# Optimization experiments

Measured on AMD Instinct MI355X. Metric: run time of the kernel, lower is better.

Reference implementation:

```python
import jax, jax.numpy as jnp
import numpy as np

BETA = 0.99  # EMA momentum from init_kwargs
EPS = 1e-12  # torch F.normalize eps


def _normalize(v):
    # matches torch.nn.functional.normalize (L2, dim=-1, eps clamp)
    n = jnp.maximum(jnp.linalg.norm(v, axis=-1, keepdims=True), EPS)
    return v / n


def setup_inputs() -> dict:
    key = jax.random.key(0)
    k1, k2 = jax.random.split(key)
    x = jax.random.normal(k1, (16384, 1024), dtype=jnp.float32)
    group_features = jax.random.uniform(k2, (8192, 1024), dtype=jnp.float32)
    return {"x": x, "group_features": group_features}


def reference(x, group_features):
    n_groups = group_features.shape[0]
    # assign_groups: cosine-sim argmax (normalized copies; does NOT modify x used below)
    xn = _normalize(x)
    gn = _normalize(group_features)
    logits = xn @ gn.T                      # [B, G]
    assignments = jnp.argmax(logits, axis=-1)  # [B] int

    # bincount over groups
    counts = jax.ops.segment_sum(
        jnp.ones_like(assignments, dtype=jnp.int32), assignments, num_segments=n_groups
    )  # [G]

    # scale only groups that received at least one sample by beta
    gf = jnp.where((counts > 0)[:, None], group_features * BETA, group_features)

    # scatter-add EMA contribution: (1-beta) * mean-style sum of raw x per group
    per_sample = x / counts[assignments][:, None].astype(x.dtype)  # safe: count>=1 for assigned
    contrib = jax.ops.segment_sum(per_sample, assignments, num_segments=n_groups)  # [G, D]
    gf = gf + (1.0 - BETA) * contrib

    return _normalize(gf)
```

## Files before the change

### kernel.cpp

```cpp
#include <hip/hip_runtime.h>
#include <float.h>

#define B_N 16384
#define G_N 8192
#define D_N 1024
#define NT 96

typedef unsigned short u16;
typedef unsigned long long u64;
typedef __attribute__((ext_vector_type(8))) short short8;
typedef __attribute__((ext_vector_type(16))) float f32x16;

#define AS1 __attribute__((address_space(1)))
#define AS3 __attribute__((address_space(3)))


__global__ __launch_bounds__(256) void k_norms(const float* __restrict__ g,
                                               float* __restrict__ invn) {
    const int j = blockIdx.x;
    const int t = threadIdx.x;
    const float4 v = *reinterpret_cast<const float4*>(&g[(size_t)j * D_N + t * 4]);
    float s = v.x * v.x + v.y * v.y + v.z * v.z + v.w * v.w;
#pragma unroll
    for (int off = 32; off >= 1; off >>= 1) s += __shfl_down(s, off, 64);
    __shared__ float wsum[4];
    if ((t & 63) == 0) wsum[t >> 6] = s;
    __syncthreads();
    if (t == 0) {
        const float tot = wsum[0] + wsum[1] + wsum[2] + wsum[3];
        invn[j] = 1.0f / fmaxf(sqrtf(tot), 1e-12f);
    }
}

__global__ void k_counts(const u64* __restrict__ pk, int* __restrict__ counts) {
    const int i = blockIdx.x * blockDim.x + threadIdx.x;
    if (i < B_N) {
        const int a = 8191 - (int)(pk[i] & 0x1FFFull);
        atomicAdd(&counts[a], 1);
    }
}

__global__ __launch_bounds__(256) void k_scatter(const float* __restrict__ x,
                                                 const u64* __restrict__ pk,
                                                 const int* __restrict__ counts,
                                                 float* __restrict__ contrib) {
    const int i = blockIdx.x;
    const int a = 8191 - (int)(pk[i] & 0x1FFFull);
    const float scale = 1.0f / (float)counts[a];
    const int t = threadIdx.x;
    const float4 v = *reinterpret_cast<const float4*>(&x[(size_t)i * D_N + t * 4]);
    float* dst = &contrib[(size_t)a * D_N + t * 4];
    atomicAdd(dst + 0, v.x * scale);
    atomicAdd(dst + 1, v.y * scale);
    atomicAdd(dst + 2, v.z * scale);
    atomicAdd(dst + 3, v.w * scale);
}

__global__ __launch_bounds__(256) void k_finalize(const float* __restrict__ g,
                                                  const int* __restrict__ counts,
                                                  float* __restrict__ out) {
    const int j = blockIdx.x;
    const int t = threadIdx.x;
    const float sc = (counts[j] > 0) ? 0.99f : 1.0f;
    const float4 gv = *reinterpret_cast<const float4*>(&g[(size_t)j * D_N + t * 4]);
    const float4 cv = *reinterpret_cast<const float4*>(&out[(size_t)j * D_N + t * 4]);
    float4 gf;
    gf.x = sc * gv.x + 0.01f * cv.x;
    gf.y = sc * gv.y + 0.01f * cv.y;
    gf.z = sc * gv.z + 0.01f * cv.z;
    gf.w = sc * gv.w + 0.01f * cv.w;
    float s = gf.x * gf.x + gf.y * gf.y + gf.z * gf.z + gf.w * gf.w;
#pragma unroll
    for (int off = 32; off >= 1; off >>= 1) s += __shfl_down(s, off, 64);
    __shared__ float wsum[4];
    __shared__ float s_inv;
    if ((t & 63) == 0) wsum[t >> 6] = s;
    __syncthreads();
    if (t == 0) s_inv = 1.0f / fmaxf(sqrtf(wsum[0] + wsum[1] + wsum[2] + wsum[3]), 1e-12f);
    __syncthreads();
    gf.x *= s_inv; gf.y *= s_inv; gf.z *= s_inv; gf.w *= s_inv;
    *reinterpret_cast<float4*>(&out[(size_t)j * D_N + t * 4]) = gf;
}


__device__ inline u16 f2bf_rtn(float f) {
    unsigned u = __float_as_uint(f);
    unsigned r = u + 0x7fffu + ((u >> 16) & 1u);
    return (u16)(r >> 16);
}
__device__ inline float bf2f(u16 h) { return __uint_as_float(((unsigned)h) << 16); }

__global__ __launch_bounds__(256) void k_split(const float* __restrict__ src,
                                               u16* __restrict__ hi,
                                               u16* __restrict__ lo) {
    const size_t i4 = (size_t)blockIdx.x * 256 + threadIdx.x;
    const float4 v = *reinterpret_cast<const float4*>(&src[i4 * 4]);
    u16 h[4], l[4];
    const float f[4] = {v.x, v.y, v.z, v.w};
#pragma unroll
    for (int j = 0; j < 4; ++j) {
        h[j] = f2bf_rtn(f[j]);
        l[j] = f2bf_rtn(f[j] - bf2f(h[j]));
    }
    *reinterpret_cast<ushort4*>(&hi[i4 * 4]) = make_ushort4(h[0], h[1], h[2], h[3]);
    *reinterpret_cast<ushort4*>(&lo[i4 * 4]) = make_ushort4(l[0], l[1], l[2], l[3]);
}


#define PHASE(T, BUF, SBUF) do {                                                          \
    const u16* base = lds + (BUF) * 16384;                                                \
    short8 afr[4][2], bfr[2][2];                                                          \
    _Pragma("unroll")                                                                     \
    for (int m = 0; m < 4; ++m) {                                                         \
        afr[m][0] = *reinterpret_cast<const short8*>(base + arow + m * 1024 + aoffk0);    \
        afr[m][1] = *reinterpret_cast<const short8*>(base + arow + m * 1024 + aoffk1);    \
    }                                                                                     \
    _Pragma("unroll")                                                                     \
    for (int n = 0; n < 2; ++n) {                                                         \
        bfr[n][0] = *reinterpret_cast<const short8*>(base + brow + n * 1024 + aoffk0);    \
        bfr[n][1] = *reinterpret_cast<const short8*>(base + brow + n * 1024 + aoffk1);    \
    }                                                                                     \
    STG((T) + 2, SBUF);                                                                   \
    __builtin_amdgcn_s_setprio(1);                                                        \
    _Pragma("unroll")                                                                     \
    for (int ks = 0; ks < 2; ++ks)                                                        \
        _Pragma("unroll")                                                                 \
        for (int m = 0; m < 4; ++m)                                                       \
            _Pragma("unroll")                                                             \
            for (int n = 0; n < 2; ++n)                                                   \
                acc[m][n] = __builtin_amdgcn_mfma_f32_32x32x16_bf16(                      \
                    afr[m][ks], bfr[n][ks], acc[m][n], 0, 0, 0);                          \
    __builtin_amdgcn_s_setprio(0);                                                        \
    asm volatile("s_waitcnt vmcnt(4)" ::: "memory");                                      \
    __builtin_amdgcn_s_barrier();                                                         \
} while (0)

__global__ __launch_bounds__(512, 2) void k_gemm_argmax(
    const u16* __restrict__ x_hi, const u16* __restrict__ x_lo,
    const u16* __restrict__ g_hi, const u16* __restrict__ g_lo,
    const float* __restrict__ invn, u64* __restrict__ pk) {

    __shared__ __align__(16) u16 lds[49152];

    const int bid = blockIdx.x;
    const int xcd = bid & 7, lcl = bid >> 3;
    const int mblk = xcd * 8 + ((lcl >> 3) & 7);
    const int nblk = (lcl & 7) + (lcl >> 6) * 8;
    const int mrow0 = mblk * 256, nrow0 = nblk * 256;

    const int tid = threadIdx.x;
    const int lane = tid & 63;
    const int w = tid >> 6;
    const int wr = w >> 2, wc = w & 3;

    const int l31 = lane & 31, l5 = lane >> 5;
    const int xq = (lane >> 1) & 3;
    const int arow = (wr * 128 + l31) * 32;
    const int brow = 8192 + (wc * 64 + l31) * 32;
    const int aoffk0 = ((0 + l5) ^ xq) * 8;
    const int aoffk1 = ((2 + l5) ^ xq) * 8;

    const int r0 = tid >> 2;
    const int xsl = (tid & 3) ^ ((tid >> 3) & 3);
    const size_t sA = (size_t)(mrow0 + r0) * D_N + xsl * 8;
    const size_t sB = (size_t)(nrow0 + r0) * D_N + xsl * 8;
    const int dstc = (tid & 448) * 8;

    auto STG = [&](int T, int buf3) {
        const int Tc = T < NT ? T : NT - 1;
        const int term = Tc >> 5;
        const u16* xb = (term == 1) ? x_lo : x_hi;
        const u16* gb = (term == 2) ? g_lo : g_hi;
        const int ko = (Tc & 31) * 32;
        u16* da = lds + buf3 * 16384;
        u16* db = da + 8192;
        __builtin_amdgcn_global_load_lds((const AS1 void*)(xb + sA + ko),          (AS3 void*)(da + dstc), 16, 0, 0);
        __builtin_amdgcn_global_load_lds((const AS1 void*)(xb + sA + 131072 + ko), (AS3 void*)(da + 4096 + dstc), 16, 0, 0);
        __builtin_amdgcn_global_load_lds((const AS1 void*)(gb + sB + ko),          (AS3 void*)(db + dstc), 16, 0, 0);
        __builtin_amdgcn_global_load_lds((const AS1 void*)(gb + sB + 131072 + ko), (AS3 void*)(db + 4096 + dstc), 16, 0, 0);
    };

    f32x16 acc[4][2];
#pragma unroll
    for (int m = 0; m < 4; ++m)
#pragma unroll
        for (int n = 0; n < 2; ++n)
#pragma unroll
            for (int r = 0; r < 16; ++r) acc[m][n][r] = 0.0f;

    STG(0, 0); STG(1, 1);
    asm volatile("s_waitcnt vmcnt(4)" ::: "memory");
    __builtin_amdgcn_s_barrier();

    for (int it = 0; it < 32; ++it) {
        const int T = it * 3;
        PHASE(T,     0, 2);
        PHASE(T + 1, 1, 0);
        PHASE(T + 2, 2, 1);
    }

    float inv[2];
    inv[0] = invn[nrow0 + wc * 64 + l31];
    inv[1] = invn[nrow0 + wc * 64 + 32 + l31];

#pragma unroll
    for (int m = 0; m < 4; ++m) {
#pragma unroll
        for (int r = 0; r < 16; ++r) {
            u64 p = 0;
#pragma unroll
            for (int n = 0; n < 2; ++n) {
                const float v = acc[m][n][r] * inv[n];
                unsigned u = __float_as_uint(v);
                u ^= (u >> 31) ? 0xFFFFFFFFu : 0x80000000u;
                const int col = nrow0 + wc * 64 + n * 32 + l31;
                const u64 cand = ((u64)u << 13) | (unsigned)(8191 - col);
                p = (cand > p) ? cand : p;
            }
#pragma unroll
            for (int msk = 1; msk < 32; msk <<= 1) {
                const u64 o = __shfl_xor(p, msk, 64);
                p = (o > p) ? o : p;
            }
            if (l31 == 0) {
                const int row = mrow0 + wr * 128 + m * 32 + (r & 3) + 8 * (r >> 2) + 4 * l5;
                atomicMax(&pk[row], p);
            }
        }
    }
}


__global__ __launch_bounds__(256) void k_argmax_fp32(const float* __restrict__ x,
                                                     const float* __restrict__ g,
                                                     const float* __restrict__ invn,
                                                     int* __restrict__ assign) {
    __shared__ __align__(16) float As[32][68];
    __shared__ __align__(16) float Bs[32][68];
    const int t = threadIdx.x;
    const int tx = t & 15;
    const int ty = t >> 4;
    const int row0 = blockIdx.x * 64;
    const int r_a = t >> 3;
    const int c4 = t & 7;
    float bestv[4]; int besti[4];
#pragma unroll
    for (int i = 0; i < 4; ++i) { bestv[i] = -3.0e38f; besti[i] = 0; }
    for (int jt = 0; jt < G_N / 64; ++jt) {
        float acc[4][4] = {};
        for (int kt = 0; kt < D_N / 32; ++kt) {
#pragma unroll
            for (int p = 0; p < 2; ++p) {
                const int r = r_a + p * 32;
                const float4 va = *reinterpret_cast<const float4*>(&x[(size_t)(row0 + r) * D_N + kt * 32 + c4 * 4]);
                As[c4 * 4 + 0][r] = va.x; As[c4 * 4 + 1][r] = va.y; As[c4 * 4 + 2][r] = va.z; As[c4 * 4 + 3][r] = va.w;
                const float4 vb = *reinterpret_cast<const float4*>(&g[(size_t)(jt * 64 + r) * D_N + kt * 32 + c4 * 4]);
                Bs[c4 * 4 + 0][r] = vb.x; Bs[c4 * 4 + 1][r] = vb.y; Bs[c4 * 4 + 2][r] = vb.z; Bs[c4 * 4 + 3][r] = vb.w;
            }
            __syncthreads();
#pragma unroll
            for (int k = 0; k < 32; ++k) {
                const float4 a = *reinterpret_cast<const float4*>(&As[k][ty * 4]);
                const float4 b = *reinterpret_cast<const float4*>(&Bs[k][tx * 4]);
                const float av[4] = {a.x, a.y, a.z, a.w};
                const float bv[4] = {b.x, b.y, b.z, b.w};
#pragma unroll
                for (int i = 0; i < 4; ++i)
#pragma unroll
                    for (int jj = 0; jj < 4; ++jj) acc[i][jj] += av[i] * bv[jj];
            }
            __syncthreads();
        }
#pragma unroll
        for (int jj = 0; jj < 4; ++jj) {
            const int col = jt * 64 + tx * 4 + jj;
            const float s = invn[col];
#pragma unroll
            for (int i = 0; i < 4; ++i) {
                const float v = acc[i][jj] * s;
                if (v > bestv[i]) { bestv[i] = v; besti[i] = col; }
            }
        }
    }
#pragma unroll
    for (int m = 1; m < 16; m <<= 1) {
#pragma unroll
        for (int i = 0; i < 4; ++i) {
            const float ov = __shfl_xor(bestv[i], m, 64);
            const int oi = __shfl_xor(besti[i], m, 64);
            if (ov > bestv[i] || (ov == bestv[i] && oi < besti[i])) { bestv[i] = ov; besti[i] = oi; }
        }
    }
    if (tx == 0) {
#pragma unroll
        for (int i = 0; i < 4; ++i) assign[row0 + ty * 4 + i] = besti[i];
    }
}

__global__ void k_counts_i(const int* __restrict__ assign, int* __restrict__ counts) {
    const int i = blockIdx.x * blockDim.x + threadIdx.x;
    if (i < B_N) atomicAdd(&counts[assign[i]], 1);
}

__global__ __launch_bounds__(256) void k_scatter_i(const float* __restrict__ x,
                                                   const int* __restrict__ assign,
                                                   const int* __restrict__ counts,
                                                   float* __restrict__ contrib) {
    const int i = blockIdx.x;
    const int a = assign[i];
    const float scale = 1.0f / (float)counts[a];
    const int t = threadIdx.x;
    const float4 v = *reinterpret_cast<const float4*>(&x[(size_t)i * D_N + t * 4]);
    float* dst = &contrib[(size_t)a * D_N + t * 4];
    atomicAdd(dst + 0, v.x * scale);
    atomicAdd(dst + 1, v.y * scale);
    atomicAdd(dst + 2, v.z * scale);
    atomicAdd(dst + 3, v.w * scale);
}


extern "C" void kernel_launch(void* const* d_in, const int* in_sizes, int n_in,
                              void* d_out, int out_size, void* d_ws, size_t ws_size,
                              hipStream_t stream) {
    const float* x = (const float*)d_in[0];
    const float* g = (const float*)d_in[1];
    float* out = (float*)d_out;

    char* ws = (char*)d_ws;
    u16*  x_hi  = (u16*)(ws);
    u16*  x_lo  = (u16*)(ws + 33554432);
    u16*  g_hi  = (u16*)(ws + 67108864);
    u16*  g_lo  = (u16*)(ws + 83886080);
    float* invn = (float*)(ws + 100663296);
    int* counts = (int*)(ws + 100696064);
    u64*   pk   = (u64*)(ws + 100728832);
    const size_t need = 100859904;

    hipMemsetAsync(out, 0, (size_t)G_N * D_N * sizeof(float), stream);

    if (ws_size >= need) {
        hipMemsetAsync(counts, 0, (size_t)G_N * sizeof(int), stream);
        hipMemsetAsync(pk, 0, (size_t)B_N * sizeof(u64), stream);
        k_norms<<<G_N, 256, 0, stream>>>(g, invn);
        k_split<<<B_N * D_N / 4 / 256, 256, 0, stream>>>(x, x_hi, x_lo);
        k_split<<<G_N * D_N / 4 / 256, 256, 0, stream>>>(g, g_hi, g_lo);
        k_gemm_argmax<<<2048, 512, 0, stream>>>(x_hi, x_lo, g_hi, g_lo, invn, pk);
        k_counts<<<B_N / 256, 256, 0, stream>>>(pk, counts);
        k_scatter<<<B_N, 256, 0, stream>>>(x, pk, counts, out);
        k_finalize<<<G_N, 256, 0, stream>>>(g, counts, out);
    } else {
        float* invn_f = (float*)ws;
        int* assign_f = (int*)(ws + (size_t)G_N * 4);
        int* counts_f = (int*)(ws + (size_t)(G_N + B_N) * 4);
        hipMemsetAsync(counts_f, 0, (size_t)G_N * sizeof(int), stream);
        k_norms<<<G_N, 256, 0, stream>>>(g, invn_f);
        k_argmax_fp32<<<B_N / 64, 256, 0, stream>>>(x, g, invn_f, assign_f);
        k_counts_i<<<B_N / 256, 256, 0, stream>>>(assign_f, counts_f);
        k_scatter_i<<<B_N, 256, 0, stream>>>(x, assign_f, counts_f, out);
        k_finalize<<<G_N, 256, 0, stream>>>(g, counts_f, out);
    }
}
```

Before: 1.107 ms.

## Pre-pack bf16 split operands into MFMA fragment order and double-buffer register reads

The hi/lo bf16 split kernel now writes its output in 32-row by 32-k bricks already arranged in MFMA lane order. Each GEMM tile stage can then be fetched with contiguous 16-byte loads, and LDS fragment reads need no swizzle arithmetic. The main loop is restructured to read fragments for the next stage into a second register set while the current stage's MFMAs run. It now waits on vmcnt(0) before each barrier, which trades some prefetch slack for the overlap and uses more registers.

```diff
diff --git a/kernel.cpp b/kernel.cpp
--- a/kernel.cpp
+++ b/kernel.cpp
@@ -1,5 +1,4 @@
 #include <hip/hip_runtime.h>
-#include <float.h>
 
 #define B_N 16384
 #define G_N 8192
@@ -90,49 +89,65 @@
 }
 __device__ inline float bf2f(u16 h) { return __uint_as_float(((unsigned)h) << 16); }
 
-__global__ __launch_bounds__(256) void k_split(const float* __restrict__ src,
-                                               u16* __restrict__ hi,
-                                               u16* __restrict__ lo) {
-    const size_t i4 = (size_t)blockIdx.x * 256 + threadIdx.x;
-    const float4 v = *reinterpret_cast<const float4*>(&src[i4 * 4]);
-    u16 h[4], l[4];
-    const float f[4] = {v.x, v.y, v.z, v.w};
-#pragma unroll
-    for (int j = 0; j < 4; ++j) {
-        h[j] = f2bf_rtn(f[j]);
-        l[j] = f2bf_rtn(f[j] - bf2f(h[j]));
-    }
-    *reinterpret_cast<ushort4*>(&hi[i4 * 4]) = make_ushort4(h[0], h[1], h[2], h[3]);
-    *reinterpret_cast<ushort4*>(&lo[i4 * 4]) = make_ushort4(l[0], l[1], l[2], l[3]);
-}
-
-
-#define PHASE(T, BUF, SBUF) do {                                                          \
-    const u16* base = lds + (BUF) * 16384;                                                \
-    short8 afr[4][2], bfr[2][2];                                                          \
-    _Pragma("unroll")                                                                     \
-    for (int m = 0; m < 4; ++m) {                                                         \
-        afr[m][0] = *reinterpret_cast<const short8*>(base + arow + m * 1024 + aoffk0);    \
-        afr[m][1] = *reinterpret_cast<const short8*>(base + arow + m * 1024 + aoffk1);    \
-    }                                                                                     \
-    _Pragma("unroll")                                                                     \
-    for (int n = 0; n < 2; ++n) {                                                         \
-        bfr[n][0] = *reinterpret_cast<const short8*>(base + brow + n * 1024 + aoffk0);    \
-        bfr[n][1] = *reinterpret_cast<const short8*>(base + brow + n * 1024 + aoffk1);    \
-    }                                                                                     \
-    STG((T) + 2, SBUF);                                                                   \
-    __builtin_amdgcn_s_setprio(1);                                                        \
-    _Pragma("unroll")                                                                     \
-    for (int ks = 0; ks < 2; ++ks)                                                        \
-        _Pragma("unroll")                                                                 \
-        for (int m = 0; m < 4; ++m)                                                       \
-            _Pragma("unroll")                                                             \
-            for (int n = 0; n < 2; ++n)                                                   \
-                acc[m][n] = __builtin_amdgcn_mfma_f32_32x32x16_bf16(                      \
-                    afr[m][ks], bfr[n][ks], acc[m][n], 0, 0, 0);                          \
-    __builtin_amdgcn_s_setprio(0);                                                        \
-    asm volatile("s_waitcnt vmcnt(4)" ::: "memory");                                      \
-    __builtin_amdgcn_s_barrier();                                                         \
+__global__ __launch_bounds__(256) void k_split_pack(const float* __restrict__ src,
+                                                    u16* __restrict__ hi,
+                                                    u16* __restrict__ lo) {
+    const int id = blockIdx.x * 256 + threadIdx.x;
+    const int brick = id >> 7, c = id & 127;
+    const int mu = brick >> 5, tau = brick & 31;
+    const int ks = c >> 6, lane = c & 63;
+    const int row = mu * 32 + (lane & 31);
+    const int k = tau * 32 + ks * 16 + (lane >> 5) * 8;
+    const float* s = src + (size_t)row * D_N + k;
+    const float4 v0 = *reinterpret_cast<const float4*>(s);
+    const float4 v1 = *reinterpret_cast<const float4*>(s + 4);
+    const float f[8] = {v0.x, v0.y, v0.z, v0.w, v1.x, v1.y, v1.z, v1.w};
+    short8 h, l;
+#pragma unroll
+    for (int j = 0; j < 8; ++j) {
+        const u16 hj = f2bf_rtn(f[j]);
+        h[j] = (short)hj;
+        l[j] = (short)f2bf_rtn(f[j] - bf2f(hj));
+    }
+    *reinterpret_cast<short8*>(hi + (size_t)id * 8) = h;
+    *reinterpret_cast<short8*>(lo + (size_t)id * 8) = l;
+}
+
+
+#define MFMA_BLK(S) do {                                                                   \
+    __builtin_amdgcn_s_setprio(1);                                                         \
+    _Pragma("unroll")                                                                      \
+    for (int ks = 0; ks < 2; ++ks)                                                         \
+        _Pragma("unroll")                                                                  \
+        for (int m = 0; m < 4; ++m)                                                        \
+            _Pragma("unroll")                                                              \
+            for (int n = 0; n < 2; ++n)                                                    \
+                acc[m][n] = __builtin_amdgcn_mfma_f32_32x32x16_bf16(                       \
+                    afr[S][m][ks], bfr[S][n][ks], acc[m][n], 0, 0, 0);                     \
+    __builtin_amdgcn_s_setprio(0);                                                         \
+} while (0)
+
+#define READS(BUF, S) do {                                                                 \
+    const u16* aB = lds + (BUF) * 16384 + aRd;                                             \
+    const u16* bB = lds + (BUF) * 16384 + 8192 + bRd;                                      \
+    _Pragma("unroll")                                                                      \
+    for (int m = 0; m < 4; ++m)                                                            \
+        _Pragma("unroll")                                                                  \
+        for (int ks = 0; ks < 2; ++ks)                                                     \
+            afr[S][m][ks] = *reinterpret_cast<const short8*>(aB + m * 1024 + ks * 512);    \
+    _Pragma("unroll")                                                                      \
+    for (int n = 0; n < 2; ++n)                                                            \
+        _Pragma("unroll")                                                                  \
+        for (int ks = 0; ks < 2; ++ks)                                                     \
+            bfr[S][n][ks] = *reinterpret_cast<const short8*>(bB + n * 1024 + ks * 512);    \
+} while (0)
+
+#define BODY(P, BSTG, BRD, SM, SR) do {                                                    \
+    asm volatile("s_waitcnt vmcnt(0)" ::: "memory");                                       \
+    __builtin_amdgcn_s_barrier();                                                          \
+    STG((P) + 2, BSTG);                                                                    \
+    READS(BRD, SR);                                                                        \
+    MFMA_BLK(SM);                                                                          \
 } while (0)
 
 __global__ __launch_bounds__(512, 2) void k_gemm_argmax(
@@ -152,32 +167,29 @@
     const int lane = tid & 63;
     const int w = tid >> 6;
     const int wr = w >> 2, wc = w & 3;
-
     const int l31 = lane & 31, l5 = lane >> 5;
-    const int xq = (lane >> 1) & 3;
-    const int arow = (wr * 128 + l31) * 32;
-    const int brow = 8192 + (wc * 64 + l31) * 32;
-    const int aoffk0 = ((0 + l5) ^ xq) * 8;
-    const int aoffk1 = ((2 + l5) ^ xq) * 8;
-
-    const int r0 = tid >> 2;
-    const int xsl = (tid & 3) ^ ((tid >> 3) & 3);
-    const size_t sA = (size_t)(mrow0 + r0) * D_N + xsl * 8;
-    const size_t sB = (size_t)(nrow0 + r0) * D_N + xsl * 8;
-    const int dstc = (tid & 448) * 8;
-
-    auto STG = [&](int T, int buf3) {
+
+    const int aRd = (wr * 512 + lane) * 8;
+    const int bRd = (wc * 256 + lane) * 8;
+
+    const int wub = (tid & 448) * 8;
+    const int cOff = (tid & 127) * 8;
+    const int brkA = tid >> 7;
+    const size_t aBase = ((size_t)(mblk * 8 + brkA)) * 32768 + cOff;
+    const size_t bBase = ((size_t)(nblk * 8 + brkA)) * 32768 + cOff;
+
+    auto STG = [&](int T, int buf) {
         const int Tc = T < NT ? T : NT - 1;
         const int term = Tc >> 5;
-        const u16* xb = (term == 1) ? x_lo : x_hi;
-        const u16* gb = (term == 2) ? g_lo : g_hi;
-        const int ko = (Tc & 31) * 32;
-        u16* da = lds + buf3 * 16384;
+        const int tko = (Tc & 31) * 1024;
+        const u16* xa = ((term == 1) ? x_lo : x_hi) + aBase + tko;
+        const u16* gb = ((term == 2) ? g_lo : g_hi) + bBase + tko;
+        u16* da = lds + buf * 16384 + wub;
         u16* db = da + 8192;
-        __builtin_amdgcn_global_load_lds((const AS1 void*)(xb + sA + ko),          (AS3 void*)(da + dstc), 16, 0, 0);
-        __builtin_amdgcn_global_load_lds((const AS1 void*)(xb + sA + 131072 + ko), (AS3 void*)(da + 4096 + dstc), 16, 0, 0);
-        __builtin_amdgcn_global_load_lds((const AS1 void*)(gb + sB + ko),          (AS3 void*)(db + dstc), 16, 0, 0);
-        __builtin_amdgcn_global_load_lds((const AS1 void*)(gb + sB + 131072 + ko), (AS3 void*)(db + 4096 + dstc), 16, 0, 0);
+        __builtin_amdgcn_global_load_lds((const AS1 void*)xa,            (AS3 void*)da, 16, 0, 0);
+        __builtin_amdgcn_global_load_lds((const AS1 void*)(xa + 131072), (AS3 void*)(da + 4096), 16, 0, 0);
+        __builtin_amdgcn_global_load_lds((const AS1 void*)gb,            (AS3 void*)db, 16, 0, 0);
+        __builtin_amdgcn_global_load_lds((const AS1 void*)(gb + 131072), (AS3 void*)(db + 4096), 16, 0, 0);
     };
 
     f32x16 acc[4][2];
@@ -187,16 +199,22 @@
         for (int n = 0; n < 2; ++n)
 #pragma unroll
             for (int r = 0; r < 16; ++r) acc[m][n][r] = 0.0f;
+
+    short8 afr[2][4][2], bfr[2][2][2];
 
     STG(0, 0); STG(1, 1);
     asm volatile("s_waitcnt vmcnt(4)" ::: "memory");
     __builtin_amdgcn_s_barrier();
-
-    for (int it = 0; it < 32; ++it) {
-        const int T = it * 3;
-        PHASE(T,     0, 2);
-        PHASE(T + 1, 1, 0);
-        PHASE(T + 2, 2, 1);
+    READS(0, 0);
+
+    for (int it = 0; it < 16; ++it) {
+        const int p = it * 6;
+        BODY(p,     2, 1, 0, 1);
+        BODY(p + 1, 0, 2, 1, 0);
+        BODY(p + 2, 1, 0, 0, 1);
+        BODY(p + 3, 2, 1, 1, 0);
+        BODY(p + 4, 0, 2, 0, 1);
+        BODY(p + 5, 1, 0, 1, 0);
     }
 
     float inv[2];
@@ -342,8 +360,8 @@
         hipMemsetAsync(counts, 0, (size_t)G_N * sizeof(int), stream);
         hipMemsetAsync(pk, 0, (size_t)B_N * sizeof(u64), stream);
         k_norms<<<G_N, 256, 0, stream>>>(g, invn);
-        k_split<<<B_N * D_N / 4 / 256, 256, 0, stream>>>(x, x_hi, x_lo);
-        k_split<<<G_N * D_N / 4 / 256, 256, 0, stream>>>(g, g_hi, g_lo);
+        k_split_pack<<<B_N * D_N / 8 / 256, 256, 0, stream>>>(x, x_hi, x_lo);
+        k_split_pack<<<G_N * D_N / 8 / 256, 256, 0, stream>>>(g, g_hi, g_lo);
         k_gemm_argmax<<<2048, 512, 0, stream>>>(x_hi, x_lo, g_hi, g_lo, invn, pk);
         k_counts<<<B_N / 256, 256, 0, stream>>>(pk, counts);
         k_scatter<<<B_N, 256, 0, stream>>>(x, pk, counts, out);
```

Measured after the change: 1.030 ms. 1.07x faster.
